# Optimization experiments

Measured on AMD Instinct MI355X. Metric: run time of the kernel, lower is better.

The kernel has to match this reference:

```python
import jax, jax.numpy as jnp
import numpy as np

INPUT_SIZE = 9
HIDDEN = 50
OUTPUT = 1


def setup_inputs() -> dict:
    key = jax.random.key(0)
    ks = jax.random.split(key, 7)
    B, T = 4096, 512
    s_ih = 1.0 / np.sqrt(HIDDEN)
    inp = {
        "x": jax.random.normal(ks[0], (B, T, INPUT_SIZE), dtype=jnp.float32),
        # PyTorch LSTM params, gate order [i, f, g, o]
        "w_ih": jax.random.uniform(ks[1], (4 * HIDDEN, INPUT_SIZE), minval=-s_ih, maxval=s_ih, dtype=jnp.float32),
        "w_hh": jax.random.uniform(ks[2], (4 * HIDDEN, HIDDEN), minval=-s_ih, maxval=s_ih, dtype=jnp.float32),
        "b_ih": jax.random.uniform(ks[3], (4 * HIDDEN,), minval=-s_ih, maxval=s_ih, dtype=jnp.float32),
        "b_hh": jax.random.uniform(ks[4], (4 * HIDDEN,), minval=-s_ih, maxval=s_ih, dtype=jnp.float32),
        "fc_w": jax.random.uniform(ks[5], (OUTPUT, HIDDEN), minval=-s_ih, maxval=s_ih, dtype=jnp.float32),
        "fc_b": jax.random.uniform(ks[6], (OUTPUT,), minval=-s_ih, maxval=s_ih, dtype=jnp.float32),
    }
    return inp


def _lstm_last_h(x, w_ih, w_hh, b_ih, b_hh):
    B, T, _ = x.shape
    H = w_hh.shape[1]
    # Precompute input-side gate pre-activations for all timesteps: [T, B, 4H]
    x_gates = jnp.einsum("bti,gi->tbg", x, w_ih) + (b_ih + b_hh)

    def step(carry, xg):
        h, c = carry
        gates = xg + h @ w_hh.T  # [B, 4H]
        i, f, g, o = jnp.split(gates, 4, axis=-1)
        i = jax.nn.sigmoid(i)
        f = jax.nn.sigmoid(f)
        g = jnp.tanh(g)
        o = jax.nn.sigmoid(o)
        c = f * c + i * g
        h = o * jnp.tanh(c)
        return (h, c), None

    h0 = jnp.zeros((B, H), dtype=x.dtype)
    c0 = jnp.zeros((B, H), dtype=x.dtype)
    (h_last, _), _ = jax.lax.scan(step, (h0, c0), x_gates)
    return h_last


def reference(x, w_ih, w_hh, b_ih, b_hh, fc_w, fc_b):
    h_last = _lstm_last_h(x, w_ih, w_hh, b_ih, b_hh)  # [B, H]
    return h_last @ fc_w.T + fc_b  # [B, 1]
```

## Files before the change

kernel.cpp:

```cpp
#include <hip/hip_runtime.h>
#include <hip/hip_bf16.h>

#define TT    512
#define ISZ   9
#define HH    50
#define NB    16
#define NWAVE 16
#define NTH   (NWAVE * 64)
#define KDIM  64

typedef _Float16 f16x8_t __attribute__((ext_vector_type(8)));
typedef float    f32x4_t __attribute__((ext_vector_type(4)));

#define L2E    1.44269504088896340736f
#define TWOL2E 2.88539008177792681472f

#define BAR() asm volatile("s_waitcnt lgkmcnt(0)\n\ts_barrier" ::: "memory")

__device__ __forceinline__ unsigned short f16h(float v) {
  _Float16 b = (_Float16)v;
  return __builtin_bit_cast(unsigned short, b);
}
__device__ __forceinline__ float sg_exp2(float z) { return __builtin_amdgcn_exp2f(z); }
__device__ __forceinline__ float rcp_f(float z)   { return __builtin_amdgcn_rcpf(z); }

__global__ __launch_bounds__(NTH, 1) void lstm_mfma(
    const float* __restrict__ x,
    const float* __restrict__ w_ih,
    const float* __restrict__ w_hh,
    const float* __restrict__ b_ih,
    const float* __restrict__ b_hh,
    const float* __restrict__ fc_w,
    const float* __restrict__ fc_b,
    float* __restrict__ out) {
  __shared__ __align__(16) unsigned short hbuf[2][NB * KDIM];
  __shared__ float redbuf[NWAVE][NB];

  const int tid = threadIdx.x;
  const int w   = tid >> 6;
  const int l   = tid & 63;
  const int lb  = l & 15;
  const int kq  = l >> 4;
  const int b0  = blockIdx.x * NB;
  const bool cw = (w < 13);

  for (int i = tid; i < (2 * NB * KDIM) / 2; i += NTH)
    reinterpret_cast<unsigned*>(hbuf)[i] = 0u;

  const int xt = tid - 13 * 64;
  const bool xact = (xt >= 0 && xt < NB * ISZ);
  const int xb = xact ? (xt / ISZ) : 0;
  const int xi = xact ? (xt - xb * ISZ) : 0;
  __syncthreads();
  if (xact) {
    float xv = x[(size_t)(b0 + xb) * (TT * ISZ) + xi];
    *(unsigned short*)((char*)hbuf[0] + (((xb << 7) + ((50 + xi) << 1)) ^ ((xb & 7) << 4))) = f16h(xv);
  }

  f16x8_t afrag[2];
  {
    const int rp   = w * 16 + lb;
    const int jA   = rp >> 2;
    const int gA   = rp & 3;
    const int rowA = gA * HH + jA;
    const bool liveA = cw && (jA < HH);
    const float scA = (gA == 2) ? TWOL2E : (-L2E);
#pragma unroll
    for (int ks = 0; ks < 2; ++ks) {
#pragma unroll
      for (int e = 0; e < 8; ++e) {
        const int K = ks * 32 + kq * 8 + e;
        float v = 0.0f;
        if (liveA) {
          if (K < HH)            v = w_hh[rowA * HH + K] * scA;
          else if (K < HH + ISZ) v = w_ih[rowA * ISZ + (K - HH)] * scA;
        }
        afrag[ks][e] = (_Float16)v;
      }
    }
  }

  const int j0 = w * 4 + kq;
  const bool live0 = cw && (j0 < HH);
  f32x4_t bias0 = {0.f, 0.f, 0.f, 0.f};
  if (live0) {
#pragma unroll
    for (int r = 0; r < 4; ++r) {
      const float sc = (r == 2) ? TWOL2E : (-L2E);
      bias0[r] = (b_ih[r * HH + j0] + b_hh[r * HH + j0]) * sc;
    }
  }

  char* const base = (char*)hbuf[0];
  const int swzb = (lb & 7) << 4;
  const int rd0 = ((lb << 7) + 0  + (kq << 4)) ^ swzb;
  const int rd1 = ((lb << 7) + 64 + (kq << 4)) ^ swzb;
  const int j0c = (j0 < HH) ? j0 : (j0 + 9);
  const int wo0 = (((lb << 7) + (j0c << 1)) ^ swzb);
  const int xwo = (((xb << 7) + ((50 + xi) << 1)) ^ ((xb & 7) << 4));

  const float* xp = x + (size_t)(b0 + xb) * (TT * ISZ) + xi;
  float csc = 0.0f, h0 = 0.0f;
  float xv_n = 0.0f;
  if (xact) xv_n = xp[ISZ];
  xp += 2 * ISZ;

#define STEP(T, ROFF, WOFF)                                                      \
  if (cw) {                                                                      \
    BAR();                                                                       \
    f16x8_t bb0 = *(const f16x8_t*)(base + rd0 + (ROFF));                        \
    f16x8_t bb1 = *(const f16x8_t*)(base + rd1 + (ROFF));                        \
    f32x4_t acc;                                                                 \
    acc = __builtin_amdgcn_mfma_f32_16x16x32_f16(afrag[0], bb0, bias0, 0,0,0);   \
    acc = __builtin_amdgcn_mfma_f32_16x16x32_f16(afrag[1], bb1, acc,   0,0,0);   \
    const float pi = sg_exp2(acc[0]);                                \
    const float pf = sg_exp2(acc[1]);                                \
    const float eg = sg_exp2(acc[2]);                                \
    const float po = sg_exp2(acc[3]);                                \
    const float A1 = 1.0f + pi, A2 = 1.0f + eg, A3 = 1.0f + pf;                  \
    const float P  = A1 * A2;                                                    \
    const float R  = rcp_f(P * A3);                                              \
    const float u  = (eg - 1.0f) * TWOL2E;                                       \
    const float fv = P * R;                                        \
    const float ig2 = u * (A3 * R);                              \
    csc = fmaf(fv, csc, ig2);                                 \
    const float ec = sg_exp2(csc);                                               \
    const float r2 = rcp_f((1.0f + po) * (1.0f + ec));                           \
    h0 = (ec - 1.0f) * r2;                                                       \
    *(unsigned short*)(base + wo0 + (WOFF)) = f16h(h0);                          \
  } else {                                                                       \
    float xv_new = 0.0f;                                                         \
    if (xact && (T) + 2 < TT) xv_new = *xp;                                      \
    xp += ISZ;                                                                   \
    BAR();                                                                       \
    if (xact && (T) + 1 < TT) *(unsigned short*)(base + xwo + (WOFF)) = f16h(xv_n); \
    xv_n = xv_new;                                                               \
  }

  for (int t2 = 0; t2 < TT; t2 += 2) {
    STEP(t2,     0x000, 0x800);
    STEP(t2 + 1, 0x800, 0x000);
  }
#undef STEP

  float p = live0 ? h0 * fc_w[j0] : 0.0f;
  p += __shfl_xor(p, 16);
  p += __shfl_xor(p, 32);
  if (l < NB) redbuf[w][l] = p;
  __syncthreads();
  if (tid < NB) {
    float a = fc_b[0];
#pragma unroll
    for (int ww = 0; ww < NWAVE; ++ww) a += redbuf[ww][tid];
    out[b0 + tid] = a;
  }
}

extern "C" void kernel_launch(void* const* d_in, const int* in_sizes, int n_in,
                              void* d_out, int out_size, void* d_ws, size_t ws_size,
                              hipStream_t stream) {
  const float* x    = (const float*)d_in[0];
  const float* w_ih = (const float*)d_in[1];
  const float* w_hh = (const float*)d_in[2];
  const float* b_ih = (const float*)d_in[3];
  const float* b_hh = (const float*)d_in[4];
  const float* fc_w = (const float*)d_in[5];
  const float* fc_b = (const float*)d_in[6];
  float* out = (float*)d_out;
  const int Btot = in_sizes[0] / (TT * ISZ);
  dim3 grid(Btot / NB), block(NTH);
  hipLaunchKernelGGL(lstm_mfma, grid, block, 0, stream,
                     x, w_ih, w_hh, b_ih, b_hh, fc_w, fc_b, out);
}
```

Baseline: 186.6 us.

## Skew LSTM hidden-unit halves across two barrier phases to overlap MFMA and gate math

Each timestep is split into two barrier-separated phases. The first MFMA, over hidden units 0–31, runs while waves 8–12 finish the cell update for units 32–49 left over from the previous step. Waves 0–7 update their cells right after the second MFMA, and the x loads and stores move into the matching phases. This overlaps half the transcendental gate math with matrix work on the recurrent critical path, at the cost of a second workgroup barrier per timestep.

Result: slower. 254.3 us (+36.3%).

```diff
diff --git a/kernel.cpp b/kernel.cpp
--- a/kernel.cpp
+++ b/kernel.cpp
@@ -23,6 +23,23 @@
 }
 __device__ __forceinline__ float sg_exp2(float z) { return __builtin_amdgcn_exp2f(z); }
 __device__ __forceinline__ float rcp_f(float z)   { return __builtin_amdgcn_rcpf(z); }
+
+__device__ __forceinline__ float cell_update(const f32x4_t acc, float& csc) {
+  const float pi = sg_exp2(acc[0]);
+  const float pf = sg_exp2(acc[1]);
+  const float eg = sg_exp2(acc[2]);
+  const float po = sg_exp2(acc[3]);
+  const float A1 = 1.0f + pi, A2 = 1.0f + eg, A3 = 1.0f + pf;
+  const float P  = A1 * A2;
+  const float R  = rcp_f(P * A3);
+  const float u  = (eg - 1.0f) * TWOL2E;
+  const float fv = P * R;
+  const float ig2 = u * (A3 * R);
+  csc = fmaf(fv, csc, ig2);
+  const float ec = sg_exp2(csc);
+  const float r2 = rcp_f((1.0f + po) * (1.0f + ec));
+  return (ec - 1.0f) * r2;
+}
 
 __global__ __launch_bounds__(NTH, 1) void lstm_mfma(
     const float* __restrict__ x,
@@ -101,47 +118,50 @@
 
   const float* xp = x + (size_t)(b0 + xb) * (TT * ISZ) + xi;
   float csc = 0.0f, h0 = 0.0f;
+  f32x4_t accP;
+  f32x4_t accB = {0.f, 0.f, 0.f, 0.f};
   float xv_n = 0.0f;
   if (xact) xv_n = xp[ISZ];
   xp += 2 * ISZ;
 
-#define STEP(T, ROFF, WOFF)                                                      \
+#define ITER(T, CUR, NXT)                                                        \
+  BAR();                                                                         \
   if (cw) {                                                                      \
-    BAR();                                                                       \
-    f16x8_t bb0 = *(const f16x8_t*)(base + rd0 + (ROFF));                        \
-    f16x8_t bb1 = *(const f16x8_t*)(base + rd1 + (ROFF));                        \
-    f32x4_t acc;                                                                 \
-    acc = __builtin_amdgcn_mfma_f32_16x16x32_f16(afrag[0], bb0, bias0, 0,0,0);   \
-    acc = __builtin_amdgcn_mfma_f32_16x16x32_f16(afrag[1], bb1, acc,   0,0,0);   \
-    const float pi = sg_exp2(acc[0]);                                \
-    const float pf = sg_exp2(acc[1]);                                \
-    const float eg = sg_exp2(acc[2]);                                \
-    const float po = sg_exp2(acc[3]);                                \
-    const float A1 = 1.0f + pi, A2 = 1.0f + eg, A3 = 1.0f + pf;                  \
-    const float P  = A1 * A2;                                                    \
-    const float R  = rcp_f(P * A3);                                              \
-    const float u  = (eg - 1.0f) * TWOL2E;                                       \
-    const float fv = P * R;                                        \
-    const float ig2 = u * (A3 * R);                              \
-    csc = fmaf(fv, csc, ig2);                                 \
-    const float ec = sg_exp2(csc);                                               \
-    const float r2 = rcp_f((1.0f + po) * (1.0f + ec));                           \
-    h0 = (ec - 1.0f) * r2;                                                       \
-    *(unsigned short*)(base + wo0 + (WOFF)) = f16h(h0);                          \
+    f16x8_t bb0 = *(const f16x8_t*)(base + rd0 + (CUR));                         \
+    if (w >= 8) {                                                                \
+      if ((T) > 0) {                                                             \
+        h0 = cell_update(accB, csc);                                             \
+        *(unsigned short*)(base + wo0 + (CUR)) = f16h(h0);                       \
+      }                                                                          \
+    }                                                                            \
+    accP = __builtin_amdgcn_mfma_f32_16x16x32_f16(afrag[0], bb0, bias0, 0,0,0);  \
+  } else {                                                                       \
+    if (xact && (T) + 1 < TT) *(unsigned short*)(base + xwo + (NXT)) = f16h(xv_n); \
+  }                                                                              \
+  BAR();                                                                         \
+  if (cw) {                                                                      \
+    f16x8_t bb1 = *(const f16x8_t*)(base + rd1 + (CUR));                         \
+    f32x4_t a2 = __builtin_amdgcn_mfma_f32_16x16x32_f16(afrag[1], bb1, accP, 0,0,0); \
+    if (w < 8) {                                                                 \
+      h0 = cell_update(a2, csc);                                                 \
+      *(unsigned short*)(base + wo0 + (NXT)) = f16h(h0);                         \
+    } else {                                                                     \
+      accB = a2;                                                                 \
+    }                                                                            \
   } else {                                                                       \
     float xv_new = 0.0f;                                                         \
     if (xact && (T) + 2 < TT) xv_new = *xp;                                      \
     xp += ISZ;                                                                   \
-    BAR();                                                                       \
-    if (xact && (T) + 1 < TT) *(unsigned short*)(base + xwo + (WOFF)) = f16h(xv_n); \
     xv_n = xv_new;                                                               \
   }
 
   for (int t2 = 0; t2 < TT; t2 += 2) {
-    STEP(t2,     0x000, 0x800);
-    STEP(t2 + 1, 0x800, 0x000);
+    ITER(t2,     0x000, 0x800);
+    ITER(t2 + 1, 0x800, 0x000);
   }
-#undef STEP
+#undef ITER
+
+  if (w >= 8 && w < 13) h0 = cell_update(accB, csc);
 
   float p = live0 ? h0 * fc_w[j0] : 0.0f;
   p += __shfl_xor(p, 16);
```

## Replace workgroup barriers with per-wave LDS flag spin-waits

Applied to the files above, without the earlier changes.

Removes the s_barrier in each recurrent step. Each wave now publishes a step counter in an LDS flag array, and consumers spin on those flags until every producer has reached the current step. The wait is split into two halves so the first MFMA can start once waves 0-7 are ready, before waves 8-15 finish. In exchange, each step pays for LDS polling, s_sleep latency and extra waitcnt fences, which may cost more than a hardware barrier.

Result: slower. 212.8 us (+14.1%).

```diff
diff --git a/kernel.cpp b/kernel.cpp
--- a/kernel.cpp
+++ b/kernel.cpp
@@ -15,14 +15,23 @@
 #define L2E    1.44269504088896340736f
 #define TWOL2E 2.88539008177792681472f
 
-#define BAR() asm volatile("s_waitcnt lgkmcnt(0)\n\ts_barrier" ::: "memory")
-
 __device__ __forceinline__ unsigned short f16h(float v) {
   _Float16 b = (_Float16)v;
   return __builtin_bit_cast(unsigned short, b);
 }
 __device__ __forceinline__ float sg_exp2(float z) { return __builtin_amdgcn_exp2f(z); }
 __device__ __forceinline__ float rcp_f(float z)   { return __builtin_amdgcn_rcpf(z); }
+
+__device__ __forceinline__ void waitge(volatile const unsigned* f, int l, unsigned thr) {
+  unsigned v = f[l & 7];
+  if (!__all((int)(v >= thr))) {
+    do {
+      __builtin_amdgcn_s_sleep(1);
+      v = f[l & 7];
+    } while (!__all((int)(v >= thr)));
+  }
+  __asm__ volatile("" ::: "memory");
+}
 
 __global__ __launch_bounds__(NTH, 1) void lstm_mfma(
     const float* __restrict__ x,
@@ -34,6 +43,7 @@
     const float* __restrict__ fc_b,
     float* __restrict__ out) {
   __shared__ __align__(16) unsigned short hbuf[2][NB * KDIM];
+  __shared__ unsigned flags[NWAVE];
   __shared__ float redbuf[NWAVE][NB];
 
   const int tid = threadIdx.x;
@@ -46,6 +56,7 @@
 
   for (int i = tid; i < (2 * NB * KDIM) / 2; i += NTH)
     reinterpret_cast<unsigned*>(hbuf)[i] = 0u;
+  if (tid < NWAVE) flags[tid] = 0u;
 
   const int xt = tid - 13 * 64;
   const bool xact = (xt >= 0 && xt < NB * ISZ);
@@ -56,6 +67,7 @@
     float xv = x[(size_t)(b0 + xb) * (TT * ISZ) + xi];
     *(unsigned short*)((char*)hbuf[0] + (((xb << 7) + ((50 + xi) << 1)) ^ ((xb & 7) << 4))) = f16h(xv);
   }
+  __syncthreads();
 
   f16x8_t afrag[2];
   {
@@ -99,42 +111,52 @@
   const int wo0 = (((lb << 7) + (j0c << 1)) ^ swzb);
   const int xwo = (((xb << 7) + ((50 + xi) << 1)) ^ ((xb & 7) << 4));
 
+  volatile unsigned* const myflag = flags + w;
+
   const float* xp = x + (size_t)(b0 + xb) * (TT * ISZ) + xi;
   float csc = 0.0f, h0 = 0.0f;
   float xv_n = 0.0f;
   if (xact) xv_n = xp[ISZ];
   xp += 2 * ISZ;
 
-#define STEP(T, ROFF, WOFF)                                                      \
-  if (cw) {                                                                      \
-    BAR();                                                                       \
-    f16x8_t bb0 = *(const f16x8_t*)(base + rd0 + (ROFF));                        \
-    f16x8_t bb1 = *(const f16x8_t*)(base + rd1 + (ROFF));                        \
-    f32x4_t acc;                                                                 \
-    acc = __builtin_amdgcn_mfma_f32_16x16x32_f16(afrag[0], bb0, bias0, 0,0,0);   \
-    acc = __builtin_amdgcn_mfma_f32_16x16x32_f16(afrag[1], bb1, acc,   0,0,0);   \
-    const float pi = sg_exp2(acc[0]);                                \
-    const float pf = sg_exp2(acc[1]);                                \
-    const float eg = sg_exp2(acc[2]);                                \
-    const float po = sg_exp2(acc[3]);                                \
-    const float A1 = 1.0f + pi, A2 = 1.0f + eg, A3 = 1.0f + pf;                  \
-    const float P  = A1 * A2;                                                    \
-    const float R  = rcp_f(P * A3);                                              \
-    const float u  = (eg - 1.0f) * TWOL2E;                                       \
-    const float fv = P * R;                                        \
-    const float ig2 = u * (A3 * R);                              \
-    csc = fmaf(fv, csc, ig2);                                 \
-    const float ec = sg_exp2(csc);                                               \
-    const float r2 = rcp_f((1.0f + po) * (1.0f + ec));                           \
-    h0 = (ec - 1.0f) * r2;                                                       \
-    *(unsigned short*)(base + wo0 + (WOFF)) = f16h(h0);                          \
-  } else {                                                                       \
-    float xv_new = 0.0f;                                                         \
-    if (xact && (T) + 2 < TT) xv_new = *xp;                                      \
-    xp += ISZ;                                                                   \
-    BAR();                                                                       \
-    if (xact && (T) + 1 < TT) *(unsigned short*)(base + xwo + (WOFF)) = f16h(xv_n); \
-    xv_n = xv_new;                                                               \
+#define STEP(T, CUR, NXT)                                                        \
+  {                                                                              \
+    const unsigned thr = (unsigned)(T);                                          \
+    if (cw) {                                                                    \
+      waitge(flags, l, thr);                       \
+      f16x8_t bb0 = *(const f16x8_t*)(base + rd0 + (CUR));                       \
+      f32x4_t accP = __builtin_amdgcn_mfma_f32_16x16x32_f16(afrag[0], bb0, bias0, 0,0,0); \
+      waitge(flags + 8, l, thr);               \
+      f16x8_t bb1 = *(const f16x8_t*)(base + rd1 + (CUR));                       \
+      f32x4_t acc = __builtin_amdgcn_mfma_f32_16x16x32_f16(afrag[1], bb1, accP, 0,0,0); \
+      const float pi = sg_exp2(acc[0]);                              \
+      const float pf = sg_exp2(acc[1]);                              \
+      const float eg = sg_exp2(acc[2]);                              \
+      const float po = sg_exp2(acc[3]);                              \
+      const float A1 = 1.0f + pi, A2 = 1.0f + eg, A3 = 1.0f + pf;                \
+      const float P  = A1 * A2;                                                  \
+      const float R  = rcp_f(P * A3);                                            \
+      const float u  = (eg - 1.0f) * TWOL2E;                                     \
+      const float fv = P * R;                                      \
+      const float ig2 = u * (A3 * R);                            \
+      csc = fmaf(fv, csc, ig2);                               \
+      const float ec = sg_exp2(csc);                                             \
+      const float r2 = rcp_f((1.0f + po) * (1.0f + ec));                         \
+      h0 = (ec - 1.0f) * r2;                                                     \
+      *(unsigned short*)(base + wo0 + (NXT)) = f16h(h0);                         \
+      __asm__ volatile("s_waitcnt lgkmcnt(0)" ::: "memory");                     \
+      if (l == 0) *myflag = thr + 1u;                                            \
+    } else {                                                                     \
+      float xv_new = 0.0f;                                                       \
+      if (xact && (T) + 2 < TT) xv_new = *xp;                                    \
+      xp += ISZ;                                                                 \
+      waitge(flags, l, thr);                   \
+      waitge(flags + 8, l, thr);                                                 \
+      if (xact && (T) + 1 < TT) *(unsigned short*)(base + xwo + (NXT)) = f16h(xv_n); \
+      __asm__ volatile("s_waitcnt lgkmcnt(0)" ::: "memory");                     \
+      if (l == 0) *myflag = thr + 1u;                                            \
+      xv_n = xv_new;                                                             \
+    }                                                                            \
   }
 
   for (int t2 = 0; t2 < TT; t2 += 2) {
```

## Process two MFMA gate tiles per wave to cut wave count and barrier cost

Applied to the files above, without the earlier changes.

Waves 0-5 now each compute two 16-row gate tiles and wave 6 computes the last tile, so only 7 compute waves plus 3 x-loader waves are needed instead of 13 plus 3. The block shrinks from 16 to 10 waves, which lowers the cost of the per-timestep workgroup barrier and lets the two independent MFMA chains and cell updates in a wave overlap. The cell-state update is also rearranged so the cell state is computed with one fma and one multiply. The trade-off is a longer serial critical path per wave, since each wave now runs two cell updates per step.

Result: no change. 189.9 us (+1.8%).

```diff
diff --git a/kernel.cpp b/kernel.cpp
--- a/kernel.cpp
+++ b/kernel.cpp
@@ -5,7 +5,7 @@
 #define ISZ   9
 #define HH    50
 #define NB    16
-#define NWAVE 16
+#define NWAVE 10
 #define NTH   (NWAVE * 64)
 #define KDIM  64
 
@@ -42,12 +42,13 @@
   const int lb  = l & 15;
   const int kq  = l >> 4;
   const int b0  = blockIdx.x * NB;
-  const bool cw = (w < 13);
+  const bool cw = (w < 7);
+  const bool two = (w < 6);
 
   for (int i = tid; i < (2 * NB * KDIM) / 2; i += NTH)
     reinterpret_cast<unsigned*>(hbuf)[i] = 0u;
 
-  const int xt = tid - 13 * 64;
+  const int xt = tid - 7 * 64;
   const bool xact = (xt >= 0 && xt < NB * ISZ);
   const int xb = xact ? (xt / ISZ) : 0;
   const int xi = xact ? (xt - xb * ISZ) : 0;
@@ -57,13 +58,18 @@
     *(unsigned short*)((char*)hbuf[0] + (((xb << 7) + ((50 + xi) << 1)) ^ ((xb & 7) << 4))) = f16h(xv);
   }
 
-  f16x8_t afrag[2];
-  {
-    const int rp   = w * 16 + lb;
+  const int tA = two ? (2 * w)     : 12;
+  const int tB = two ? (2 * w + 1) : 12;
+  f16x8_t afrag[2][2];
+#pragma unroll
+  for (int tt = 0; tt < 2; ++tt) {
+    const int tile = tt ? tB : tA;
+    const bool actT = cw && (two || tt == 0);
+    const int rp   = tile * 16 + lb;
     const int jA   = rp >> 2;
     const int gA   = rp & 3;
     const int rowA = gA * HH + jA;
-    const bool liveA = cw && (jA < HH);
+    const bool liveA = actT && (jA < HH);
     const float scA = (gA == 2) ? TWOL2E : (-L2E);
 #pragma unroll
     for (int ks = 0; ks < 2; ++ks) {
@@ -75,20 +81,21 @@
           if (K < HH)            v = w_hh[rowA * HH + K] * scA;
           else if (K < HH + ISZ) v = w_ih[rowA * ISZ + (K - HH)] * scA;
         }
-        afrag[ks][e] = (_Float16)v;
+        afrag[tt][ks][e] = (_Float16)v;
       }
     }
   }
 
-  const int j0 = w * 4 + kq;
+  const int j0 = tA * 4 + kq;
+  const int j1 = tB * 4 + kq;
   const bool live0 = cw && (j0 < HH);
   f32x4_t bias0 = {0.f, 0.f, 0.f, 0.f};
-  if (live0) {
+  f32x4_t bias1 = {0.f, 0.f, 0.f, 0.f};
 #pragma unroll
-    for (int r = 0; r < 4; ++r) {
-      const float sc = (r == 2) ? TWOL2E : (-L2E);
-      bias0[r] = (b_ih[r * HH + j0] + b_hh[r * HH + j0]) * sc;
-    }
+  for (int r = 0; r < 4; ++r) {
+    const float sc = (r == 2) ? TWOL2E : (-L2E);
+    if (live0) bias0[r] = (b_ih[r * HH + j0] + b_hh[r * HH + j0]) * sc;
+    if (two)   bias1[r] = (b_ih[r * HH + j1] + b_hh[r * HH + j1]) * sc;
   }
 
   char* const base = (char*)hbuf[0];
@@ -96,44 +103,51 @@
   const int rd0 = ((lb << 7) + 0  + (kq << 4)) ^ swzb;
   const int rd1 = ((lb << 7) + 64 + (kq << 4)) ^ swzb;
   const int j0c = (j0 < HH) ? j0 : (j0 + 9);
-  const int wo0 = (((lb << 7) + (j0c << 1)) ^ swzb);
+  const int woA = (((lb << 7) + (j0c << 1)) ^ swzb);
+  const int woB = (((lb << 7) + (j1  << 1)) ^ swzb);
   const int xwo = (((xb << 7) + ((50 + xi) << 1)) ^ ((xb & 7) << 4));
 
   const float* xp = x + (size_t)(b0 + xb) * (TT * ISZ) + xi;
-  float csc = 0.0f, h0 = 0.0f;
+  float csc0 = 0.0f, h0 = 0.0f, csc1 = 0.0f, h1 = 0.0f;
   float xv_n = 0.0f;
   if (xact) xv_n = xp[ISZ];
   xp += 2 * ISZ;
 
-#define STEP(T, ROFF, WOFF)                                                      \
-  if (cw) {                                                                      \
-    BAR();                                                                       \
-    f16x8_t bb0 = *(const f16x8_t*)(base + rd0 + (ROFF));                        \
-    f16x8_t bb1 = *(const f16x8_t*)(base + rd1 + (ROFF));                        \
-    f32x4_t acc;                                                                 \
-    acc = __builtin_amdgcn_mfma_f32_16x16x32_f16(afrag[0], bb0, bias0, 0,0,0);   \
-    acc = __builtin_amdgcn_mfma_f32_16x16x32_f16(afrag[1], bb1, acc,   0,0,0);   \
-    const float pi = sg_exp2(acc[0]);                                \
-    const float pf = sg_exp2(acc[1]);                                \
-    const float eg = sg_exp2(acc[2]);                                \
-    const float po = sg_exp2(acc[3]);                                \
+#define CELL(acc, cscv, hv, wo, WOFF)                                            \
+  {                                                                              \
+    const float pi = sg_exp2(acc[0]);                                            \
+    const float pf = sg_exp2(acc[1]);                                            \
+    const float eg = sg_exp2(acc[2]);                                            \
+    const float po = sg_exp2(acc[3]);                                            \
     const float A1 = 1.0f + pi, A2 = 1.0f + eg, A3 = 1.0f + pf;                  \
     const float P  = A1 * A2;                                                    \
     const float R  = rcp_f(P * A3);                                              \
-    const float u  = (eg - 1.0f) * TWOL2E;                                       \
-    const float fv = P * R;                                        \
-    const float ig2 = u * (A3 * R);                              \
-    csc = fmaf(fv, csc, ig2);                                 \
-    const float ec = sg_exp2(csc);                                               \
+    const float t1 = fmaf(P, cscv, (eg - 1.0f) * TWOL2E * A3);                   \
+    cscv = t1 * R;                                                               \
+    const float ec = sg_exp2(cscv);                                              \
     const float r2 = rcp_f((1.0f + po) * (1.0f + ec));                           \
-    h0 = (ec - 1.0f) * r2;                                                       \
-    *(unsigned short*)(base + wo0 + (WOFF)) = f16h(h0);                          \
+    hv = (ec - 1.0f) * r2;                                                       \
+    *(unsigned short*)(base + (wo) + (WOFF)) = f16h(hv);                         \
+  }
+
+#define STEP(T, CUR, NXT)                                                        \
+  if (cw) {                                                                      \
+    BAR();                                                                       \
+    f16x8_t bb0 = *(const f16x8_t*)(base + rd0 + (CUR));                         \
+    f16x8_t bb1 = *(const f16x8_t*)(base + rd1 + (CUR));                         \
+    f32x4_t accA = __builtin_amdgcn_mfma_f32_16x16x32_f16(afrag[0][0], bb0, bias0, 0,0,0); \
+    f32x4_t accB;                                                                \
+    if (two) accB = __builtin_amdgcn_mfma_f32_16x16x32_f16(afrag[1][0], bb0, bias1, 0,0,0); \
+    accA = __builtin_amdgcn_mfma_f32_16x16x32_f16(afrag[0][1], bb1, accA, 0,0,0); \
+    if (two) accB = __builtin_amdgcn_mfma_f32_16x16x32_f16(afrag[1][1], bb1, accB, 0,0,0); \
+    CELL(accA, csc0, h0, woA, NXT);                                              \
+    if (two) CELL(accB, csc1, h1, woB, NXT);                                     \
   } else {                                                                       \
     float xv_new = 0.0f;                                                         \
     if (xact && (T) + 2 < TT) xv_new = *xp;                                      \
     xp += ISZ;                                                                   \
     BAR();                                                                       \
-    if (xact && (T) + 1 < TT) *(unsigned short*)(base + xwo + (WOFF)) = f16h(xv_n); \
+    if (xact && (T) + 1 < TT) *(unsigned short*)(base + xwo + (NXT)) = f16h(xv_n); \
     xv_n = xv_new;                                                               \
   }
 
@@ -142,8 +156,10 @@
     STEP(t2 + 1, 0x800, 0x000);
   }
 #undef STEP
+#undef CELL
 
   float p = live0 ? h0 * fc_w[j0] : 0.0f;
+  if (two) p += h1 * fc_w[j1];
   p += __shfl_xor(p, 16);
   p += __shfl_xor(p, 32);
   if (l < NB) redbuf[w][l] = p;
```
